# Kernel tuning notes

Measured on AMD Instinct MI355X. Metric: run time of the kernel, lower is better.

The kernel has to match this reference:

```python
import jax, jax.numpy as jnp
import numpy as np

N = 16384          # batch of signals
DIM_T = 256        # time steps per signal
DT = 0.01          # integration dt (intg_lev=1 -> dt_intg = dt)
NUF = 256          # num_units_feat
HID_XI = 128       # hidlayers_xi
HID_AUX = 64       # hidlayers_aux1_dec
LEN_INTG = DIM_T   # (dim_t-1)*intg_lev + 1 with intg_lev=1


def _linear_init(key, fan_in, fan_out):
    # torch nn.Linear default: U(-1/sqrt(fan_in), 1/sqrt(fan_in))
    s = 1.0 / np.sqrt(fan_in)
    kw, kb = jax.random.split(key)
    W = jax.random.uniform(kw, (fan_in, fan_out), minval=-s, maxval=s, dtype=jnp.float32)
    b = jax.random.uniform(kb, (fan_out,), minval=-s, maxval=s, dtype=jnp.float32)
    return W, b


def setup_inputs() -> dict:
    key = jax.random.key(0)
    ks = jax.random.split(key, 12)
    data = jax.random.normal(ks[0], (N, DIM_T), dtype=jnp.float32)
    omega = jax.random.normal(ks[1], (N, 1), dtype=jnp.float32)
    eps = jax.random.normal(ks[2], (N, 1), dtype=jnp.float32)
    # feature extractor (mlp branch): [dim_t+1 -> 256 -> 256], relu after both (actfun_output=True)
    W_feat1, b_feat1 = _linear_init(ks[3], DIM_T + 1, NUF)
    W_feat2, b_feat2 = _linear_init(ks[4], NUF, NUF)
    # xi mean head: MLP [256 -> 128 -> 1] then Softplus
    W_xim1, b_xim1 = _linear_init(ks[5], NUF, HID_XI)
    W_xim2, b_xim2 = _linear_init(ks[6], HID_XI, 1)
    # xi lnvar head: MLP [256 -> 128 -> 1]
    W_xil1, b_xil1 = _linear_init(ks[7], NUF, HID_XI)
    W_xil2, b_xil2 = _linear_init(ks[8], HID_XI, 1)
    # decoder aux1 MLP: [dim_z_aux1+1=2 -> 64 -> 1]
    W_aux1, b_aux1 = _linear_init(ks[9], 2, HID_AUX)
    W_aux2, b_aux2 = _linear_init(ks[10], HID_AUX, 1)
    return dict(data=data, omega=omega, eps=eps,
                W_feat1=W_feat1, b_feat1=b_feat1, W_feat2=W_feat2, b_feat2=b_feat2,
                W_xim1=W_xim1, b_xim1=b_xim1, W_xim2=W_xim2, b_xim2=b_xim2,
                W_xil1=W_xil1, b_xil1=b_xil1, W_xil2=W_xil2, b_xil2=b_xil2,
                W_aux1=W_aux1, b_aux1=b_aux1, W_aux2=W_aux2, b_aux2=b_aux2)


def reference(data, omega, eps,
              W_feat1, b_feat1, W_feat2, b_feat2,
              W_xim1, b_xim1, W_xim2, b_xim2,
              W_xil1, b_xil1, W_xil2, b_xil2,
              W_aux1, b_aux1, W_aux2, b_aux2):
    relu = jax.nn.relu
    # ---- encode_xi ----
    x_ = jnp.concatenate([data, omega], axis=1)                 # [n, dim_t+1]
    feat = relu(relu(x_ @ W_feat1 + b_feat1) @ W_feat2 + b_feat2)  # [n, 256]
    xi_mean = jax.nn.softplus(relu(feat @ W_xim1 + b_xim1) @ W_xim2 + b_xim2)  # [n, 1]
    xi_lnvar = relu(feat @ W_xil1 + b_xil1) @ W_xil2 + b_xil2                  # [n, 1]
    # ---- draw (reparameterization + clamp to feasible range [0, 1]) ----
    xi = xi_mean + jnp.exp(0.5 * xi_lnvar) * eps
    xi = jnp.clip(xi, 0.0, 1.0)
    # ---- decode: Euler odeint over LEN_INTG steps of state yy=[y, dy/dt] ----
    init_y = data[:, :1]                                        # [n, 1]
    initcond = jnp.concatenate([init_y, jnp.zeros_like(init_y)], axis=1)  # [n, 2]

    def step(yy, _):
        # physics: d[y, v]/dt = [v, 0]; aux MLP adds acceleration from (z_aux1=omega, y)
        aux_in = jnp.concatenate([omega, yy[:, :1]], axis=1)    # [n, 2]
        acc = relu(aux_in @ W_aux1 + b_aux1) @ W_aux2 + b_aux2  # [n, 1]
        dyy = jnp.concatenate([yy[:, 1:2], acc], axis=1)        # [n, 2]
        return yy + DT * dyy, yy

    _, yy_seq = jax.lax.scan(step, initcond, None, length=LEN_INTG)  # [len_intg, n, 2]
    y_seq = yy_seq[:, :, 0].T                                   # [n, dim_t] (intg_lev=1)
    t_intg = DT * jnp.arange(LEN_INTG, dtype=jnp.float32)       # [dim_t]
    x_PAB = jnp.exp(-jnp.abs(xi) * t_intg[None, :]) * y_seq     # [n, dim_t]
    return xi_mean, xi_lnvar, x_PAB
```

## Files before the change

kernel.cpp:

```cpp
#include <hip/hip_runtime.h>
#include <math.h>

#define NROWS 16384
#define DT_C 0.01f

typedef short s16x8 __attribute__((ext_vector_type(8)));
typedef float f32x4 __attribute__((ext_vector_type(4)));

__device__ __forceinline__ unsigned short f2bf(float f) {
    unsigned u = __float_as_uint(f);
    u += 0x7fffu + ((u >> 16) & 1u);
    return (unsigned short)(u >> 16);
}
__device__ __forceinline__ unsigned pack2bf(float a, float b) {
    return (unsigned)f2bf(a) | ((unsigned)f2bf(b) << 16);
}
__device__ __forceinline__ float swz1(float v){ return __int_as_float(__builtin_amdgcn_ds_swizzle(__float_as_int(v), 0x041F)); }
__device__ __forceinline__ float swz2(float v){ return __int_as_float(__builtin_amdgcn_ds_swizzle(__float_as_int(v), 0x081F)); }
__device__ __forceinline__ float swz4(float v){ return __int_as_float(__builtin_amdgcn_ds_swizzle(__float_as_int(v), 0x101F)); }

__global__ __launch_bounds__(256) void prep_k(
    const float* __restrict__ Wf1, const float* __restrict__ Wf2,
    const float* __restrict__ Wm1, const float* __restrict__ Wl1,
    const float* __restrict__ bm1, const float* __restrict__ bl1,
    unsigned short* __restrict__ wpack, float* __restrict__ biasH)
{
    const int id = blockIdx.x * 256 + threadIdx.x;
    const int n  = id & 255;
    const int k8 = (id >> 8) & 31;
    const int s  = id >> 13;

    unsigned short tmp[8];
    #pragma unroll
    for (int j = 0; j < 8; ++j) {
        const int k = k8 * 8 + j;
        float v;
        if (s == 0)      v = Wf1[k * 256 + n];
        else if (s == 1) v = Wf2[k * 256 + n];
        else             v = (n < 128) ? Wm1[k * 128 + n] : Wl1[k * 128 + n - 128];
        tmp[j] = f2bf(v);
    }
    *(uint4*)&wpack[((s * 32 + k8) * 256 + n) * 8] = *(const uint4*)tmp;

    if (id < 256) biasH[id] = (id < 128) ? bm1[id] : bl1[id - 128];
}

__global__ __launch_bounds__(256, 2) void mega_k(
    const float* __restrict__ data, const float* __restrict__ omega,
    const unsigned short* __restrict__ wpack, const float* __restrict__ biasH,
    const float* __restrict__ bf1, const float* __restrict__ bf2,
    const float* __restrict__ w256g,
    const float* __restrict__ Wm2, const float* __restrict__ bm2,
    const float* __restrict__ Wl2, const float* __restrict__ bl2,
    float* __restrict__ out_mean, float* __restrict__ out_lnvar)
{
    __shared__ unsigned short As1[8192];
    __shared__ unsigned short Hs[8192];
    __shared__ unsigned short Bs[16384];
    __shared__ float omg[32];

    const int tid  = threadIdx.x;
    const int wid  = tid >> 6;
    const int lane = tid & 63;
    const int ln   = lane & 15;
    const int quad = lane >> 4;
    const int r0   = blockIdx.x * 32;

    {
        #pragma unroll
        for (int g2 = 0; g2 < 8; ++g2) {
            const int unit = g2 * 256 + tid;
            const int m    = unit >> 6;
            const int c16  = unit & 63;
            const int kblk = c16 >> 1;
            const int h    = c16 & 1;
            const float4 v = *(const float4*)&data[(size_t)(r0 + m) * 256 + c16 * 4];
            unsigned* d = (unsigned*)&As1[((kblk * 32) + (m ^ (kblk & 7))) * 8 + h * 4];
            d[0] = pack2bf(v.x, v.y);
            d[1] = pack2bf(v.z, v.w);
        }
        if (tid < 32) omg[tid] = omega[r0 + tid];
    }

    f32x4 acc[2][4];

    auto seed = [&](const float* bias) {
        #pragma unroll
        for (int nt = 0; nt < 4; ++nt) {
            const float b = bias[wid * 64 + nt * 16 + ln];
            acc[0][nt] = f32x4{b, b, b, b};
            acc[1][nt] = acc[0][nt];
        }
    };

    auto run_stage = [&](const unsigned short* Ap, const unsigned short* wp) {
        for (int c = 0; c < 4; ++c) {
            __syncthreads();
            {
                const uint4* src = (const uint4*)(wp + c * 16384);
                uint4 tmp[8];
                #pragma unroll
                for (int i = 0; i < 8; ++i) tmp[i] = src[i * 256 + tid];
                #pragma unroll
                for (int i = 0; i < 8; ++i) ((uint4*)Bs)[i * 256 + tid] = tmp[i];
            }
            __syncthreads();
            #pragma unroll
            for (int kk = 0; kk < 2; ++kk) {
                const int kb   = kk * 4 + quad;
                const int kblk = c * 8 + kb;
                const int f    = kblk & 7;
                s16x8 a0 = *(const s16x8*)&Ap[(kblk * 32 + (ln ^ f)) * 8];
                s16x8 a1 = *(const s16x8*)&Ap[(kblk * 32 + ((ln ^ f) + 16)) * 8];
                #pragma unroll
                for (int nt = 0; nt < 4; ++nt) {
                    s16x8 b = *(const s16x8*)&Bs[(kb * 256 + wid * 64 + nt * 16 + ln) * 8];
                    acc[0][nt] = __builtin_amdgcn_mfma_f32_16x16x32_bf16(a0, b, acc[0][nt], 0, 0, 0);
                    acc[1][nt] = __builtin_amdgcn_mfma_f32_16x16x32_bf16(a1, b, acc[1][nt], 0, 0, 0);
                }
            }
        }
    };

    auto write_packed = [&](unsigned short* dst, bool addOm) {
        #pragma unroll
        for (int nt = 0; nt < 4; ++nt) {
            const int col = wid * 64 + nt * 16 + ln;
            const int kg  = col >> 3, f = kg & 7, jj = col & 7;
            const float wo = addOm ? w256g[col] : 0.f;
            #pragma unroll
            for (int mt = 0; mt < 2; ++mt) {
                #pragma unroll
                for (int r = 0; r < 4; ++r) {
                    const int row = mt * 16 + quad * 4 + r;
                    float v = acc[mt][nt][r];
                    if (addOm) v = fmaf(omg[row], wo, v);
                    v = fmaxf(v, 0.f);
                    dst[(kg * 32 + (row ^ f)) * 8 + jj] = f2bf(v);
                }
            }
        }
    };

    seed(bf1);
    run_stage(As1, wpack);
    write_packed(Hs, true);
    seed(bf2);
    run_stage(Hs, wpack + 65536);
    write_packed(As1, false);
    seed(biasH);
    run_stage(As1, wpack + 131072);
    __syncthreads();
    float* headsF = (float*)Bs;
    #pragma unroll
    for (int nt = 0; nt < 4; ++nt) {
        const int col = wid * 64 + nt * 16 + ln;
        #pragma unroll
        for (int mt = 0; mt < 2; ++mt) {
            #pragma unroll
            for (int r = 0; r < 4; ++r) {
                const int row = mt * 16 + quad * 4 + r;
                headsF[row * 256 + ((col + row * 8) & 255)] = fmaxf(acc[mt][nt][r], 0.f);
            }
        }
    }
    __syncthreads();

    {
        const int m = tid >> 3, l = tid & 7;
        float pm = 0.f, pl = 0.f;
        #pragma unroll
        for (int q = 0; q < 4; ++q) {
            const int c0 = l * 16 + q * 4;
            const float4 hm = *(const float4*)&headsF[m * 256 + ((c0 + m * 8) & 255)];
            const float4 wm = *(const float4*)&Wm2[c0];
            const float4 hl = *(const float4*)&headsF[m * 256 + ((128 + c0 + m * 8) & 255)];
            const float4 wl = *(const float4*)&Wl2[c0];
            pm = fmaf(hm.w, wm.w, fmaf(hm.z, wm.z, fmaf(hm.y, wm.y, fmaf(hm.x, wm.x, pm))));
            pl = fmaf(hl.w, wl.w, fmaf(hl.z, wl.z, fmaf(hl.y, wl.y, fmaf(hl.x, wl.x, pl))));
        }
        pm += swz1(pm); pm += swz2(pm); pm += swz4(pm);
        pl += swz1(pl); pl += swz2(pl); pl += swz4(pl);
        if (l == 0) {
            const float xm = pm + bm2[0];
            out_mean[r0 + m]  = fmaxf(xm, 0.f) + log1pf(expf(-fabsf(xm)));
            out_lnvar[r0 + m] = pl + bl2[0];
        }
    }
}

__global__ __launch_bounds__(256) void ode_k(
    const float* __restrict__ data, const float* __restrict__ omega_g,
    const float* __restrict__ eps_g,
    const float* __restrict__ W1, const float* __restrict__ b1,
    const float* __restrict__ W2, const float* __restrict__ b2p,
    const float* __restrict__ xmean, const float* __restrict__ xlnv,
    float* __restrict__ xout)
{
    const int tid = threadIdx.x;
    const int r   = tid >> 3;
    const int l   = tid & 7;
    const int row = blockIdx.x * 32 + r;

    const float4 w1a = *(const float4*)&W1[64 + l * 8];
    const float4 w1b = *(const float4*)&W1[64 + l * 8 + 4];
    const float4 w0a = *(const float4*)&W1[l * 8];
    const float4 w0b = *(const float4*)&W1[l * 8 + 4];
    const float4 bba = *(const float4*)&b1[l * 8];
    const float4 bbb = *(const float4*)&b1[l * 8 + 4];
    const float4 w2a = *(const float4*)&W2[l * 8];
    const float4 w2b = *(const float4*)&W2[l * 8 + 4];

    const float om = omega_g[row];
    const float ep = eps_g[row];
    float xi = xmean[row] + expf(0.5f * xlnv[row]) * ep;
    xi = fminf(fmaxf(xi, 0.f), 1.f);
    const float s = expf(-xi * DT_C);
    const float pseed = b2p[0] * 0.125f;

    const float A0 = fmaf(om, w0a.x, bba.x), A1 = fmaf(om, w0a.y, bba.y);
    const float A2 = fmaf(om, w0a.z, bba.z), A3 = fmaf(om, w0a.w, bba.w);
    const float A4 = fmaf(om, w0b.x, bbb.x), A5 = fmaf(om, w0b.y, bbb.y);
    const float A6 = fmaf(om, w0b.z, bbb.z), A7 = fmaf(om, w0b.w, bbb.w);

    auto partial = [&](float y) -> float {
        float h0 = fmaxf(fmaf(y, w1a.x, A0), 0.f);
        float h1 = fmaxf(fmaf(y, w1a.y, A1), 0.f);
        float h2 = fmaxf(fmaf(y, w1a.z, A2), 0.f);
        float h3 = fmaxf(fmaf(y, w1a.w, A3), 0.f);
        float h4 = fmaxf(fmaf(y, w1b.x, A4), 0.f);
        float h5 = fmaxf(fmaf(y, w1b.y, A5), 0.f);
        float h6 = fmaxf(fmaf(y, w1b.z, A6), 0.f);
        float h7 = fmaxf(fmaf(y, w1b.w, A7), 0.f);
        float pA = fmaf(h0, w2a.x, pseed);
        pA = fmaf(h1, w2a.y, pA);
        pA = fmaf(h2, w2a.z, pA);
        pA = fmaf(h3, w2a.w, pA);
        float pB = h4 * w2b.x;
        pB = fmaf(h5, w2b.y, pB);
        pB = fmaf(h6, w2b.z, pB);
        pB = fmaf(h7, w2b.w, pB);
        return pA + pB;
    };

    const float y0 = data[(size_t)row * 256];
    float ym = y0;
    float yc = y0;
    const float DT2 = DT_C * DT_C;

    float p = partial(ym);
    p += swz1(p); p += swz2(p); p += swz4(p);
    float pr = p;

    float d = 1.f;
    float* orow = xout + (size_t)row * 256 + l * 4;

    for (int tb = 0; tb < 8; ++tb) {
        float cur[4];
        #pragma unroll
        for (int j = 0; j < 32; ++j) {
            const float m_ = d * ym;
            if ((j >> 2) == l) cur[j & 3] = m_;
            d *= s;
            float pn = partial(yc);
            pn += swz1(pn); pn += swz2(pn); pn += swz4(pn);
            const float ynext = fmaf(DT2, pr, fmaf(2.f, yc, -ym));
            ym = yc; yc = ynext; pr = pn;
        }
        *(float4*)&orow[tb * 32] = *(const float4*)cur;
    }
}

extern "C" void kernel_launch(void* const* d_in, const int* in_sizes, int n_in,
                              void* d_out, int out_size, void* d_ws, size_t ws_size,
                              hipStream_t stream)
{
    const float* data    = (const float*)d_in[0];
    const float* omega   = (const float*)d_in[1];
    const float* eps     = (const float*)d_in[2];
    const float* W_feat1 = (const float*)d_in[3];
    const float* b_feat1 = (const float*)d_in[4];
    const float* W_feat2 = (const float*)d_in[5];
    const float* b_feat2 = (const float*)d_in[6];
    const float* W_xim1  = (const float*)d_in[7];
    const float* b_xim1  = (const float*)d_in[8];
    const float* W_xim2  = (const float*)d_in[9];
    const float* b_xim2  = (const float*)d_in[10];
    const float* W_xil1  = (const float*)d_in[11];
    const float* b_xil1  = (const float*)d_in[12];
    const float* W_xil2  = (const float*)d_in[13];
    const float* b_xil2  = (const float*)d_in[14];
    const float* W_aux1  = (const float*)d_in[15];
    const float* b_aux1  = (const float*)d_in[16];
    const float* W_aux2  = (const float*)d_in[17];
    const float* b_aux2  = (const float*)d_in[18];

    float* out_mean  = (float*)d_out;
    float* out_lnvar = out_mean + NROWS;
    float* out_x     = out_lnvar + NROWS;

    unsigned short* wpack = (unsigned short*)d_ws;
    float* biasH = (float*)((char*)d_ws + 3 * 32 * 256 * 8 * 2);

    prep_k<<<96, 256, 0, stream>>>(W_feat1, W_feat2, W_xim1, W_xil1,
                                   b_xim1, b_xil1, wpack, biasH);
    mega_k<<<512, 256, 0, stream>>>(data, omega, wpack, biasH,
                                    b_feat1, b_feat2, W_feat1 + 256 * 256,
                                    W_xim2, b_xim2, W_xil2, b_xil2,
                                    out_mean, out_lnvar);
    ode_k<<<512, 256, 0, stream>>>(data, omega, eps, W_aux1, b_aux1,
                                   W_aux2, b_aux2, out_mean, out_lnvar, out_x);
}
```

Before: 148.3 us.

## Fuse encoder MLP and ODE integration into one kernel, read weights from global

Merges the MLP encoder kernel and the Euler ODE kernel into a single kernel, so xi is computed in shared memory and never goes through global memory, and one launch is removed. The GEMM stages now load B fragments directly from global/L2 instead of staging them through shared memory, which drops the per-chunk syncs and the shared-memory copies. The aux MLP in the ODE loop is rewritten with packed two-wide float FMA/max. Risks: per-wave global loads of weights may add latency compared with the LDS staging, and the fused kernel's higher register and LDS use could reduce overlap between the MFMA phase and the serial ODE phase.

```diff
diff --git a/kernel.cpp b/kernel.cpp
--- a/kernel.cpp
+++ b/kernel.cpp
@@ -6,6 +6,7 @@
 
 typedef short s16x8 __attribute__((ext_vector_type(8)));
 typedef float f32x4 __attribute__((ext_vector_type(4)));
+typedef float f32x2 __attribute__((ext_vector_type(2)));
 
 __device__ __forceinline__ unsigned short f2bf(float f) {
     unsigned u = __float_as_uint(f);
@@ -45,19 +46,24 @@
     if (id < 256) biasH[id] = (id < 128) ? bm1[id] : bl1[id - 128];
 }
 
-__global__ __launch_bounds__(256, 2) void mega_k(
+__global__ __launch_bounds__(256, 2) void fused_k(
     const float* __restrict__ data, const float* __restrict__ omega,
+    const float* __restrict__ eps_g,
     const unsigned short* __restrict__ wpack, const float* __restrict__ biasH,
     const float* __restrict__ bf1, const float* __restrict__ bf2,
     const float* __restrict__ w256g,
     const float* __restrict__ Wm2, const float* __restrict__ bm2,
     const float* __restrict__ Wl2, const float* __restrict__ bl2,
-    float* __restrict__ out_mean, float* __restrict__ out_lnvar)
+    const float* __restrict__ Wa1, const float* __restrict__ ba1,
+    const float* __restrict__ Wa2, const float* __restrict__ ba2,
+    float* __restrict__ out_mean, float* __restrict__ out_lnvar,
+    float* __restrict__ xout)
 {
     __shared__ unsigned short As1[8192];
     __shared__ unsigned short Hs[8192];
-    __shared__ unsigned short Bs[16384];
+    __shared__ float headsF[32 * 256];
     __shared__ float omg[32];
+    __shared__ float xiS[32];
 
     const int tid  = threadIdx.x;
     const int wid  = tid >> 6;
@@ -94,30 +100,27 @@
     };
 
     auto run_stage = [&](const unsigned short* Ap, const unsigned short* wp) {
+        #pragma unroll
         for (int c = 0; c < 4; ++c) {
-            __syncthreads();
-            {
-                const uint4* src = (const uint4*)(wp + c * 16384);
-                uint4 tmp[8];
-                #pragma unroll
-                for (int i = 0; i < 8; ++i) tmp[i] = src[i * 256 + tid];
-                #pragma unroll
-                for (int i = 0; i < 8; ++i) ((uint4*)Bs)[i * 256 + tid] = tmp[i];
-            }
-            __syncthreads();
             #pragma unroll
             for (int kk = 0; kk < 2; ++kk) {
                 const int kb   = kk * 4 + quad;
                 const int kblk = c * 8 + kb;
                 const int f    = kblk & 7;
+                s16x8 b0 = *(const s16x8*)&wp[((size_t)(kblk * 256) + wid * 64 + 0 * 16 + ln) * 8];
+                s16x8 b1 = *(const s16x8*)&wp[((size_t)(kblk * 256) + wid * 64 + 1 * 16 + ln) * 8];
+                s16x8 b2 = *(const s16x8*)&wp[((size_t)(kblk * 256) + wid * 64 + 2 * 16 + ln) * 8];
+                s16x8 b3 = *(const s16x8*)&wp[((size_t)(kblk * 256) + wid * 64 + 3 * 16 + ln) * 8];
                 s16x8 a0 = *(const s16x8*)&Ap[(kblk * 32 + (ln ^ f)) * 8];
                 s16x8 a1 = *(const s16x8*)&Ap[(kblk * 32 + ((ln ^ f) + 16)) * 8];
-                #pragma unroll
-                for (int nt = 0; nt < 4; ++nt) {
-                    s16x8 b = *(const s16x8*)&Bs[(kb * 256 + wid * 64 + nt * 16 + ln) * 8];
-                    acc[0][nt] = __builtin_amdgcn_mfma_f32_16x16x32_bf16(a0, b, acc[0][nt], 0, 0, 0);
-                    acc[1][nt] = __builtin_amdgcn_mfma_f32_16x16x32_bf16(a1, b, acc[1][nt], 0, 0, 0);
-                }
+                acc[0][0] = __builtin_amdgcn_mfma_f32_16x16x32_bf16(a0, b0, acc[0][0], 0, 0, 0);
+                acc[1][0] = __builtin_amdgcn_mfma_f32_16x16x32_bf16(a1, b0, acc[1][0], 0, 0, 0);
+                acc[0][1] = __builtin_amdgcn_mfma_f32_16x16x32_bf16(a0, b1, acc[0][1], 0, 0, 0);
+                acc[1][1] = __builtin_amdgcn_mfma_f32_16x16x32_bf16(a1, b1, acc[1][1], 0, 0, 0);
+                acc[0][2] = __builtin_amdgcn_mfma_f32_16x16x32_bf16(a0, b2, acc[0][2], 0, 0, 0);
+                acc[1][2] = __builtin_amdgcn_mfma_f32_16x16x32_bf16(a1, b2, acc[1][2], 0, 0, 0);
+                acc[0][3] = __builtin_amdgcn_mfma_f32_16x16x32_bf16(a0, b3, acc[0][3], 0, 0, 0);
+                acc[1][3] = __builtin_amdgcn_mfma_f32_16x16x32_bf16(a1, b3, acc[1][3], 0, 0, 0);
             }
         }
     };
@@ -142,16 +145,17 @@
         }
     };
 
+    __syncthreads();
     seed(bf1);
     run_stage(As1, wpack);
     write_packed(Hs, true);
+    __syncthreads();
     seed(bf2);
     run_stage(Hs, wpack + 65536);
     write_packed(As1, false);
+    __syncthreads();
     seed(biasH);
     run_stage(As1, wpack + 131072);
-    __syncthreads();
-    float* headsF = (float*)Bs;
     #pragma unroll
     for (int nt = 0; nt < 4; ++nt) {
         const int col = wid * 64 + nt * 16 + ln;
@@ -182,92 +186,74 @@
         pm += swz1(pm); pm += swz2(pm); pm += swz4(pm);
         pl += swz1(pl); pl += swz2(pl); pl += swz4(pl);
         if (l == 0) {
-            const float xm = pm + bm2[0];
-            out_mean[r0 + m]  = fmaxf(xm, 0.f) + log1pf(expf(-fabsf(xm)));
-            out_lnvar[r0 + m] = pl + bl2[0];
-        }
-    }
-}
-
-__global__ __launch_bounds__(256) void ode_k(
-    const float* __restrict__ data, const float* __restrict__ omega_g,
-    const float* __restrict__ eps_g,
-    const float* __restrict__ W1, const float* __restrict__ b1,
-    const float* __restrict__ W2, const float* __restrict__ b2p,
-    const float* __restrict__ xmean, const float* __restrict__ xlnv,
-    float* __restrict__ xout)
-{
-    const int tid = threadIdx.x;
-    const int r   = tid >> 3;
-    const int l   = tid & 7;
-    const int row = blockIdx.x * 32 + r;
-
-    const float4 w1a = *(const float4*)&W1[64 + l * 8];
-    const float4 w1b = *(const float4*)&W1[64 + l * 8 + 4];
-    const float4 w0a = *(const float4*)&W1[l * 8];
-    const float4 w0b = *(const float4*)&W1[l * 8 + 4];
-    const float4 bba = *(const float4*)&b1[l * 8];
-    const float4 bbb = *(const float4*)&b1[l * 8 + 4];
-    const float4 w2a = *(const float4*)&W2[l * 8];
-    const float4 w2b = *(const float4*)&W2[l * 8 + 4];
-
-    const float om = omega_g[row];
-    const float ep = eps_g[row];
-    float xi = xmean[row] + expf(0.5f * xlnv[row]) * ep;
-    xi = fminf(fmaxf(xi, 0.f), 1.f);
-    const float s = expf(-xi * DT_C);
-    const float pseed = b2p[0] * 0.125f;
-
-    const float A0 = fmaf(om, w0a.x, bba.x), A1 = fmaf(om, w0a.y, bba.y);
-    const float A2 = fmaf(om, w0a.z, bba.z), A3 = fmaf(om, w0a.w, bba.w);
-    const float A4 = fmaf(om, w0b.x, bbb.x), A5 = fmaf(om, w0b.y, bbb.y);
-    const float A6 = fmaf(om, w0b.z, bbb.z), A7 = fmaf(om, w0b.w, bbb.w);
-
-    auto partial = [&](float y) -> float {
-        float h0 = fmaxf(fmaf(y, w1a.x, A0), 0.f);
-        float h1 = fmaxf(fmaf(y, w1a.y, A1), 0.f);
-        float h2 = fmaxf(fmaf(y, w1a.z, A2), 0.f);
-        float h3 = fmaxf(fmaf(y, w1a.w, A3), 0.f);
-        float h4 = fmaxf(fmaf(y, w1b.x, A4), 0.f);
-        float h5 = fmaxf(fmaf(y, w1b.y, A5), 0.f);
-        float h6 = fmaxf(fmaf(y, w1b.z, A6), 0.f);
-        float h7 = fmaxf(fmaf(y, w1b.w, A7), 0.f);
-        float pA = fmaf(h0, w2a.x, pseed);
-        pA = fmaf(h1, w2a.y, pA);
-        pA = fmaf(h2, w2a.z, pA);
-        pA = fmaf(h3, w2a.w, pA);
-        float pB = h4 * w2b.x;
-        pB = fmaf(h5, w2b.y, pB);
-        pB = fmaf(h6, w2b.z, pB);
-        pB = fmaf(h7, w2b.w, pB);
-        return pA + pB;
-    };
-
-    const float y0 = data[(size_t)row * 256];
-    float ym = y0;
-    float yc = y0;
-    const float DT2 = DT_C * DT_C;
-
-    float p = partial(ym);
-    p += swz1(p); p += swz2(p); p += swz4(p);
-    float pr = p;
-
-    float d = 1.f;
-    float* orow = xout + (size_t)row * 256 + l * 4;
-
-    for (int tb = 0; tb < 8; ++tb) {
-        float cur[4];
-        #pragma unroll
-        for (int j = 0; j < 32; ++j) {
-            const float m_ = d * ym;
-            if ((j >> 2) == l) cur[j & 3] = m_;
-            d *= s;
-            float pn = partial(yc);
-            pn += swz1(pn); pn += swz2(pn); pn += swz4(pn);
-            const float ynext = fmaf(DT2, pr, fmaf(2.f, yc, -ym));
-            ym = yc; yc = ynext; pr = pn;
-        }
-        *(float4*)&orow[tb * 32] = *(const float4*)cur;
+            const float xm  = pm + bm2[0];
+            const float mean = fmaxf(xm, 0.f) + log1pf(expf(-fabsf(xm)));
+            const float lnv  = pl + bl2[0];
+            out_mean[r0 + m]  = mean;
+            out_lnvar[r0 + m] = lnv;
+            float xi = mean + expf(0.5f * lnv) * eps_g[r0 + m];
+            xiS[m] = fminf(fmaxf(xi, 0.f), 1.f);
+        }
+    }
+    __syncthreads();
+
+    {
+        const int r   = tid >> 3;
+        const int l   = tid & 7;
+        const int row = r0 + r;
+        const float om = omg[r];
+        const float xi = xiS[r];
+        const float s  = expf(-xi * DT_C);
+        const float pseed = ba2[0] * 0.125f;
+
+        f32x2 w1v[4], Av[4], w2v[4];
+        #pragma unroll
+        for (int i = 0; i < 4; ++i) {
+            const f32x2 w0 = *(const f32x2*)&Wa1[l * 8 + i * 2];
+            const f32x2 bb = *(const f32x2*)&ba1[l * 8 + i * 2];
+            w1v[i] = *(const f32x2*)&Wa1[64 + l * 8 + i * 2];
+            w2v[i] = *(const f32x2*)&Wa2[l * 8 + i * 2];
+            Av[i]  = f32x2{fmaf(om, w0.x, bb.x), fmaf(om, w0.y, bb.y)};
+        }
+
+        auto partial = [&](float y) -> float {
+            const f32x2 y2 = f32x2{y, y};
+            f32x2 acc2 = f32x2{pseed, 0.f};
+            #pragma unroll
+            for (int i = 0; i < 4; ++i) {
+                f32x2 h = __builtin_elementwise_fma(y2, w1v[i], Av[i]);
+                h = __builtin_elementwise_max(h, f32x2{0.f, 0.f});
+                acc2 = __builtin_elementwise_fma(h, w2v[i], acc2);
+            }
+            return acc2.x + acc2.y;
+        };
+
+        const float y0 = data[(size_t)row * 256];
+        float ym = y0;
+        float yc = y0;
+        const float DT2 = DT_C * DT_C;
+
+        float p = partial(ym);
+        p += swz1(p); p += swz2(p); p += swz4(p);
+        float pr = p;
+
+        float d = 1.f;
+        float* orow = xout + (size_t)row * 256 + l * 4;
+
+        for (int tb = 0; tb < 8; ++tb) {
+            float cur[4];
+            #pragma unroll
+            for (int j = 0; j < 32; ++j) {
+                const float m_ = d * ym;
+                if ((j >> 2) == l) cur[j & 3] = m_;
+                d *= s;
+                float pn = partial(yc);
+                pn += swz1(pn); pn += swz2(pn); pn += swz4(pn);
+                const float ynext = fmaf(DT2, pr, fmaf(2.f, yc, -ym));
+                ym = yc; yc = ynext; pr = pn;
+            }
+            *(float4*)&orow[tb * 32] = *(const float4*)cur;
+        }
     }
 }
 
@@ -304,10 +290,9 @@
 
     prep_k<<<96, 256, 0, stream>>>(W_feat1, W_feat2, W_xim1, W_xil1,
                                    b_xim1, b_xil1, wpack, biasH);
-    mega_k<<<512, 256, 0, stream>>>(data, omega, wpack, biasH,
-                                    b_feat1, b_feat2, W_feat1 + 256 * 256,
-                                    W_xim2, b_xim2, W_xil2, b_xil2,
-                                    out_mean, out_lnvar);
-    ode_k<<<512, 256, 0, stream>>>(data, omega, eps, W_aux1, b_aux1,
-                                   W_aux2, b_aux2, out_mean, out_lnvar, out_x);
-}
+    fused_k<<<512, 256, 0, stream>>>(data, omega, eps, wpack, biasH,
+                                     b_feat1, b_feat2, W_feat1 + 256 * 256,
+                                     W_xim2, b_xim2, W_xil2, b_xil2,
+                                     W_aux1, b_aux1, W_aux2, b_aux2,
+                                     out_mean, out_lnvar, out_x);
+}
```

After: 145.7 us. No clear change (-1.7%).
